# Kernel tuning notes

Measured on AMD Instinct MI355X. Metric: run time of the kernel, lower is better.

Reference implementation:

```python
import jax, jax.numpy as jnp
import numpy as np

D = 512        # d_model
DFF = 2048     # d_ffn
H = 8          # n_heads
L = 4          # n_blocks
EPS = 1e-5     # nn.LayerNorm default eps
NEG = -1e9


def _layer_norm(x, g, b):
    m = jnp.mean(x, axis=-1, keepdims=True)
    v = jnp.var(x, axis=-1, keepdims=True)
    return (x - m) / jnp.sqrt(v + EPS) * g + b


def setup_inputs() -> dict:
    key = jax.random.key(0)
    ks = jax.random.split(key, 6)
    B, S = 2, 2048
    s = 0.02
    x = jax.random.normal(ks[0], (B, S, D), dtype=jnp.float32)
    Wq = jax.random.normal(ks[1], (L, D, D), dtype=jnp.float32) * s
    Wk = jax.random.normal(ks[2], (L, D, D), dtype=jnp.float32) * s
    Wv = jax.random.normal(ks[3], (L, D, D), dtype=jnp.float32) * s
    W1 = jax.random.normal(ks[4], (L, D, DFF), dtype=jnp.float32) * s
    W2 = jax.random.normal(ks[5], (L, DFF, D), dtype=jnp.float32) * s
    z_d = jnp.zeros((L, D), dtype=jnp.float32)
    o_d = jnp.ones((L, D), dtype=jnp.float32)
    return {
        'x': x,
        'Wq': Wq, 'bq': z_d, 'Wk': Wk, 'bk': z_d, 'Wv': Wv, 'bv': z_d,
        'W1': W1, 'b1': jnp.zeros((L, DFF), dtype=jnp.float32),
        'W2': W2, 'b2': z_d,
        'g1': o_d, 'beta1': z_d, 'g2': o_d, 'beta2': z_d,
    }


def reference(x, Wq, bq, Wk, bk, Wv, bv, W1, b1, W2, b2, g1, beta1, g2, beta2):
    B, S, Dm = x.shape
    dk = Dm // H
    scale = 1.0 / (dk ** 0.5)

    def block(h, p):
        wq, bq_, wk, bk_, wv, bv_, w1, b1_, w2, b2_, g1_, be1, g2_, be2 = p
        # QKV projections, split heads: [B,S,D] -> [B,H,S,dk]
        q = (h @ wq + bq_).reshape(B, S, H, dk).transpose(0, 2, 1, 3)
        k = (h @ wk + bk_).reshape(B, S, H, dk).transpose(0, 2, 1, 3)
        v = (h @ wv + bv_).reshape(B, S, H, dk).transpose(0, 2, 1, 3)
        scores = jnp.einsum('bhqd,bhkd->bhqk', q, k) * scale
        # original quirk: padding=0, scores exactly equal to 0 get masked to -1e9
        scores = jnp.where(scores != 0, scores, NEG)
        probs = jax.nn.softmax(scores, axis=-1)
        attn = jnp.einsum('bhqk,bhkd->bhqd', probs, v)
        attn = attn.transpose(0, 2, 1, 3).reshape(B, S, Dm)
        h = _layer_norm(attn + h, g1_, be1)           # add_and_norm1
        ff = jax.nn.relu(h @ w1 + b1_) @ w2 + b2_     # position-wise FFN
        h = _layer_norm(h + ff, g2_, be2)             # add_and_norm2
        return h, None

    params = (Wq, bq, Wk, bk, Wv, bv, W1, b1, W2, b2, g1, beta1, g2, beta2)
    out, _ = jax.lax.scan(block, x, params)
    return out
```

## Files before the change

### kernel.cpp

```cpp
#include <hip/hip_runtime.h>
#include <stdint.h>
#include <math.h>


typedef __bf16 bf16_t;
typedef bf16_t bf16x8 __attribute__((ext_vector_type(8)));
typedef bf16_t bf16x4v __attribute__((ext_vector_type(4)));
typedef float  f32x4  __attribute__((ext_vector_type(4)));

__device__ __forceinline__ f32x4 mfma16(bf16x8 a, bf16x8 b, f32x4 c) {
    return __builtin_amdgcn_mfma_f32_16x16x32_bf16(a, b, c, 0, 0, 0);
}

__device__ __forceinline__ void cp16(const void* g, const void* l) {
    auto gp = reinterpret_cast<const __attribute__((address_space(1))) char*>(
        reinterpret_cast<uintptr_t>(g));
    auto lp = reinterpret_cast<__attribute__((address_space(3))) char*>(
        static_cast<uint32_t>(reinterpret_cast<uintptr_t>(l)));
    __builtin_amdgcn_global_load_lds((const __attribute__((address_space(1))) void*)gp,
                                     (__attribute__((address_space(3))) void*)lp,
                                     16, 0, 0);
}

__global__ void wconv_kernel(const float* __restrict__ Wq, const float* __restrict__ Wk,
                             const float* __restrict__ Wv, const float* __restrict__ W1,
                             const float* __restrict__ W2,
                             bf16_t* __restrict__ oQKV, bf16_t* __restrict__ oW1,
                             bf16_t* __restrict__ oW2)
{
    const int l = blockIdx.y;
    int t = blockIdx.x;
    const float* in; bf16_t* out; int Kd, Nd, tt;
    if (t < 192) {
        int m = t / 64; tt = t % 64; Kd = 512; Nd = 512;
        in  = (m == 0 ? Wq : m == 1 ? Wk : Wv) + (size_t)l * 512 * 512;
        out = oQKV + (size_t)l * 1536 * 512 + (size_t)m * 512 * 512;
    } else if (t < 448) {
        tt = t - 192; Kd = 512; Nd = 2048;
        in  = W1 + (size_t)l * 512 * 2048;
        out = oW1 + (size_t)l * 2048 * 512;
    } else {
        tt = t - 448; Kd = 2048; Nd = 512;
        in  = W2 + (size_t)l * 2048 * 512;
        out = oW2 + (size_t)l * 512 * 2048;
    }
    const int ntx = Nd >> 6;
    const int bk = (tt / ntx) * 64, bn = (tt % ntx) * 64;
    __shared__ float tile[64][65];
    const int tid = threadIdx.x;
    #pragma unroll
    for (int i = 0; i < 16; ++i) {
        int idx = i * 256 + tid; int r = idx >> 6, c = idx & 63;
        tile[r][c] = in[(size_t)(bk + r) * Nd + bn + c];
    }
    __syncthreads();
    #pragma unroll
    for (int i = 0; i < 4; ++i) {
        int idx = i * 256 + tid; int n = idx >> 4, kc = (idx & 15) * 4;
        bf16x4v o;
        o[0] = (bf16_t)tile[kc + 0][n];
        o[1] = (bf16_t)tile[kc + 1][n];
        o[2] = (bf16_t)tile[kc + 2][n];
        o[3] = (bf16_t)tile[kc + 3][n];
        *(bf16x4v*)&out[(size_t)(bn + n) * Kd + bk + kc] = o;
    }
}

__global__ void f2b_kernel(const float* __restrict__ in, bf16_t* __restrict__ out, int n)
{
    int i = (blockIdx.x * 256 + threadIdx.x) * 8;
    if (i >= n) return;
    float4 a = *(const float4*)(in + i);
    float4 b = *(const float4*)(in + i + 4);
    bf16x8 o;
    o[0] = (bf16_t)a.x; o[1] = (bf16_t)a.y; o[2] = (bf16_t)a.z; o[3] = (bf16_t)a.w;
    o[4] = (bf16_t)b.x; o[5] = (bf16_t)b.y; o[6] = (bf16_t)b.z; o[7] = (bf16_t)b.w;
    *(bf16x8*)(out + i) = o;
}

template<int MODE, bool RELU>
__global__ __launch_bounds__(256, 4) void gemm_kernel(
    const bf16_t* __restrict__ A, const bf16_t* __restrict__ Wt,
    const float* __restrict__ b0, const float* __restrict__ b1, const float* __restrict__ b2,
    void* __restrict__ o0, void* __restrict__ o1, void* __restrict__ o2,
    int N, int lda, int klen)
{
    __shared__ __align__(16) bf16_t lA[2][128 * 32];
    __shared__ __align__(16) bf16_t lB[2][128 * 32];
    const int tid = threadIdx.x;
    const int lane = tid & 63, w = tid >> 6;
    const int wm = w >> 1, wn = w & 1;
    const int l15 = lane & 15, quad = lane >> 4;
    const int row0 = blockIdx.y * 128, col0 = blockIdx.x * 128;
    const int kst = blockIdx.z * klen, kend = kst + klen;
    const int wbase = (tid & 192) * 16;

    f32x4 acc[4][4] = {};
    const char* Ab = (const char*)A;
    const char* Bb = (const char*)Wt;

    auto stage = [&](int k0, int buf) {
        #pragma unroll
        for (int p = 0; p < 2; ++p) {
            int o = (p * 256 + tid) * 16;
            int r = o >> 6, cb = o & 63;
            cp16(Ab + ((size_t)(row0 + r) * lda + k0) * 2 + cb, (char*)lA[buf] + p * 4096 + wbase);
            cp16(Bb + ((size_t)(col0 + r) * lda + k0) * 2 + cb, (char*)lB[buf] + p * 4096 + wbase);
        }
    };

    stage(kst, 0);
    int it = 0;
    for (int k0 = kst; k0 < kend; k0 += 32, ++it) {
        __syncthreads();
        if (k0 + 32 < kend) stage(k0 + 32, (it + 1) & 1);
        const bf16_t* cA = lA[it & 1];
        const bf16_t* cB = lB[it & 1];
        bf16x8 af[4], bv_[4];
        #pragma unroll
        for (int i = 0; i < 4; ++i)
            af[i] = *(const bf16x8*)&cA[(wm * 64 + i * 16 + l15) * 32 + quad * 8];
        #pragma unroll
        for (int i = 0; i < 4; ++i)
            bv_[i] = *(const bf16x8*)&cB[(wn * 64 + i * 16 + l15) * 32 + quad * 8];
        #pragma unroll
        for (int mi = 0; mi < 4; ++mi)
            #pragma unroll
            for (int ni = 0; ni < 4; ++ni)
                acc[mi][ni] = mfma16(af[mi], bv_[ni], acc[mi][ni]);
    }

    #pragma unroll
    for (int mi = 0; mi < 4; ++mi) {
        const int rowb = row0 + wm * 64 + mi * 16 + quad * 4;
        #pragma unroll
        for (int ni = 0; ni < 4; ++ni) {
            const int col = col0 + wn * 64 + ni * 16 + l15;
            if (MODE == 1) {
                const float bias = b0[col];
                #pragma unroll
                for (int r = 0; r < 4; ++r) {
                    float v = acc[mi][ni][r] + bias;
                    if (RELU) v = fmaxf(v, 0.f);
                    ((bf16_t*)o0)[(size_t)(rowb + r) * N + col] = (bf16_t)v;
                }
            } else if (MODE == 3) {
                bf16_t* op = (bf16_t*)o0 + (size_t)blockIdx.z * 4096 * 512;
                #pragma unroll
                for (int r = 0; r < 4; ++r)
                    op[(size_t)(rowb + r) * N + col] = (bf16_t)acc[mi][ni][r];
            } else {
                if (col < 512) {
                    const float bias = b0[col];
                    #pragma unroll
                    for (int r = 0; r < 4; ++r)
                        ((bf16_t*)o0)[(size_t)(rowb + r) * 512 + col] =
                            (bf16_t)((acc[mi][ni][r] + bias) * 0.18033688f);
                } else if (col < 1024) {
                    const int c = col - 512;
                    const float bias = b1[c];
                    #pragma unroll
                    for (int r = 0; r < 4; ++r)
                        ((bf16_t*)o1)[(size_t)(rowb + r) * 512 + c] =
                            (bf16_t)(acc[mi][ni][r] + bias);
                } else {
                    const int cv = col - 1024;
                    const int hh = cv >> 6, d = cv & 63;
                    const float bias = b2[cv];
                    const int b_ = rowb >> 11, s = rowb & 2047;
                    bf16x4v pk;
                    #pragma unroll
                    for (int r = 0; r < 4; ++r)
                        pk[r] = (bf16_t)(acc[mi][ni][r] + bias);
                    *(bf16x4v*)&((bf16_t*)o2)[(size_t)((b_ * 8 + hh) * 64 + d) * 2048 + s] = pk;
                }
            }
        }
    }
}

__global__ __launch_bounds__(256, 7) void attn_kernel(
    const bf16_t* __restrict__ Q, const bf16_t* __restrict__ Kg,
    const bf16_t* __restrict__ Vt, bf16_t* __restrict__ Op,
    float* __restrict__ Lb)
{
    __shared__ __align__(16) bf16_t lK[2][64 * 32];
    __shared__ __align__(16) bf16_t lV[2][64 * 32];
    __shared__ __align__(16) bf16_t lP[4][576];
    const int tid = threadIdx.x;
    const int lane = tid & 63, w = tid >> 6;
    const int l15 = lane & 15, quad = lane >> 4;
    const int bh = blockIdx.y, b = bh >> 3, h = bh & 7;
    const int q0 = blockIdx.x * 64;
    const int sp = blockIdx.z, kbase = sp * 512;
    const int wbase = w * 1024;
    const int srow = tid >> 2, scb = (tid & 3) * 16;

    bf16x8 qf[2];
    #pragma unroll
    for (int ks = 0; ks < 2; ++ks)
        qf[ks] = *(const bf16x8*)&Q[(size_t)(b * 2048 + q0 + w * 16 + l15) * 512
                                     + h * 64 + ks * 32 + quad * 8];

    f32x4 oaccT[4] = {};
    float tsum[4] = {0.f, 0.f, 0.f, 0.f};

    for (int t = 0; t < 8; ++t) {
        const int k0 = kbase + t * 64;
        __syncthreads();
        #pragma unroll
        for (int ks = 0; ks < 2; ++ks)
            cp16((const char*)Kg + ((size_t)(b * 2048 + k0 + srow) * 512 + h * 64 + ks * 32) * 2 + scb,
                 (char*)lK[ks] + wbase);
        #pragma unroll
        for (int g = 0; g < 2; ++g)
            cp16((const char*)Vt + ((size_t)(bh * 64 + srow) * 2048 + k0 + g * 32) * 2 + scb,
                 (char*)lV[g] + wbase);
        __syncthreads();

        f32x4 sacc[4] = {};
        #pragma unroll
        for (int ni = 0; ni < 4; ++ni) {
            bf16x8 kf0 = *(const bf16x8*)&lK[0][(ni * 16 + l15) * 32 + quad * 8];
            bf16x8 kf1 = *(const bf16x8*)&lK[1][(ni * 16 + l15) * 32 + quad * 8];
            sacc[ni] = mfma16(qf[0], kf0, sacc[ni]);
            sacc[ni] = mfma16(qf[1], kf1, sacc[ni]);
        }

        #pragma unroll
        for (int ni = 0; ni < 4; ++ni)
            #pragma unroll
            for (int r = 0; r < 4; ++r) {
                float s = sacc[ni][r];
                float p_ = (s == 0.f) ? 0.f : __builtin_amdgcn_exp2f(s);
                sacc[ni][r] = p_;
                tsum[r] += p_;
            }

        #pragma unroll
        for (int kc = 0; kc < 2; ++kc) {
            #pragma unroll
            for (int nn = 0; nn < 2; ++nn) {
                const int ni = kc * 2 + nn;
                #pragma unroll
                for (int r = 0; r < 4; ++r)
                    lP[w][(quad * 4 + r) * 36 + nn * 16 + l15] = (bf16_t)sacc[ni][r];
            }
            bf16x4v p0 = *(const bf16x4v*)&lP[w][l15 * 36 + quad * 8];
            bf16x4v p1 = *(const bf16x4v*)&lP[w][l15 * 36 + quad * 8 + 4];
            bf16x8 pf;
            #pragma unroll
            for (int j = 0; j < 4; ++j) { pf[j] = p0[j]; pf[4 + j] = p1[j]; }
            #pragma unroll
            for (int nd = 0; nd < 4; ++nd) {
                bf16x8 vf = *(const bf16x8*)&lV[kc][(nd * 16 + l15) * 32 + quad * 8];
                oaccT[nd] = mfma16(vf, pf, oaccT[nd]);
            }
        }
    }

    #pragma unroll
    for (int r = 0; r < 4; ++r) {
        float s_ = tsum[r];
        s_ += __shfl_xor(s_, 1);
        s_ += __shfl_xor(s_, 2);
        s_ += __shfl_xor(s_, 4);
        s_ += __shfl_xor(s_, 8);
        tsum[r] = s_;
    }

    bf16_t* op = Op + (size_t)sp * 4096 * 512;
    {
        const int row = b * 2048 + q0 + w * 16 + l15;
        #pragma unroll
        for (int nd = 0; nd < 4; ++nd) {
            bf16x4v pk;
            #pragma unroll
            for (int r = 0; r < 4; ++r) pk[r] = (bf16_t)oaccT[nd][r];
            *(bf16x4v*)&op[(size_t)row * 512 + h * 64 + nd * 16 + quad * 4] = pk;
        }
    }
    if (l15 == 0) {
        #pragma unroll
        for (int r = 0; r < 4; ++r) {
            int row = b * 2048 + q0 + w * 16 + quad * 4 + r;
            Lb[((size_t)row * 8 + h) * 4 + sp] = tsum[r];
        }
    }
}

__global__ void lnadd_c(const bf16_t* __restrict__ Op, const float* __restrict__ Lb,
                        const float* __restrict__ hin,
                        const float* __restrict__ g, const float* __restrict__ be,
                        float* __restrict__ Yf, bf16_t* __restrict__ Yb)
{
    const int row = blockIdx.x * 4 + (threadIdx.x >> 6);
    const int lane = threadIdx.x & 63;
    const int c0 = lane * 8;
    const int head = lane >> 3;
    const float4 l4 = *(const float4*)&Lb[((size_t)row * 8 + head) * 4];
    const float linv = 1.f / (l4.x + l4.y + l4.z + l4.w);
    const size_t idx = (size_t)row * 512 + c0;
    bf16x8 o0 = *(const bf16x8*)&Op[idx];
    bf16x8 o1 = *(const bf16x8*)&Op[idx + 2097152];
    bf16x8 o2 = *(const bf16x8*)&Op[idx + 2 * 2097152];
    bf16x8 o3 = *(const bf16x8*)&Op[idx + 3 * 2097152];
    float4 h0 = *(const float4*)&hin[idx];
    float4 h1 = *(const float4*)&hin[idx + 4];
    const float hr[8] = {h0.x, h0.y, h0.z, h0.w, h1.x, h1.y, h1.z, h1.w};
    float v[8]; float s = 0.f;
    #pragma unroll
    for (int j = 0; j < 8; ++j) {
        v[j] = ((float)o0[j] + (float)o1[j] + (float)o2[j] + (float)o3[j]) * linv + hr[j];
        s += v[j];
    }
    #pragma unroll
    for (int off = 32; off >= 1; off >>= 1) s += __shfl_xor(s, off);
    const float mean = s * (1.f / 512.f);
    float vs = 0.f;
    #pragma unroll
    for (int j = 0; j < 8; ++j) { float d = v[j] - mean; vs += d * d; }
    #pragma unroll
    for (int off = 32; off >= 1; off >>= 1) vs += __shfl_xor(vs, off);
    const float inv = rsqrtf(vs * (1.f / 512.f) + 1e-5f);
    float4 g0 = *(const float4*)&g[c0], g1 = *(const float4*)&g[c0 + 4];
    float4 b0 = *(const float4*)&be[c0], b1 = *(const float4*)&be[c0 + 4];
    const float gg[8] = {g0.x, g0.y, g0.z, g0.w, g1.x, g1.y, g1.z, g1.w};
    const float bb[8] = {b0.x, b0.y, b0.z, b0.w, b1.x, b1.y, b1.z, b1.w};
    float y[8]; bf16x8 yb;
    #pragma unroll
    for (int j = 0; j < 8; ++j) {
        y[j] = (v[j] - mean) * inv * gg[j] + bb[j];
        yb[j] = (bf16_t)y[j];
    }
    *(float4*)&Yf[idx]     = make_float4(y[0], y[1], y[2], y[3]);
    *(float4*)&Yf[idx + 4] = make_float4(y[4], y[5], y[6], y[7]);
    *(bf16x8*)&Yb[idx] = yb;
}

__global__ void lnadd_f(const bf16_t* __restrict__ G, const float* __restrict__ bias,
                        const float* __restrict__ hres, const float* __restrict__ g,
                        const float* __restrict__ be,
                        float* __restrict__ Yf, bf16_t* __restrict__ Yb)
{
    const int row = blockIdx.x * 4 + (threadIdx.x >> 6);
    const int lane = threadIdx.x & 63;
    const int c0 = lane * 8;
    const size_t idx = (size_t)row * 512 + c0;
    bf16x8 o0 = *(const bf16x8*)&G[idx];
    bf16x8 o1 = *(const bf16x8*)&G[idx + 2097152];
    bf16x8 o2 = *(const bf16x8*)&G[idx + 2 * 2097152];
    bf16x8 o3 = *(const bf16x8*)&G[idx + 3 * 2097152];
    float4 h0 = *(const float4*)&hres[idx];
    float4 h1 = *(const float4*)&hres[idx + 4];
    float4 bi0 = *(const float4*)&bias[c0], bi1 = *(const float4*)&bias[c0 + 4];
    const float hr[8] = {h0.x, h0.y, h0.z, h0.w, h1.x, h1.y, h1.z, h1.w};
    const float bs[8] = {bi0.x, bi0.y, bi0.z, bi0.w, bi1.x, bi1.y, bi1.z, bi1.w};
    float v[8]; float s = 0.f;
    #pragma unroll
    for (int j = 0; j < 8; ++j) {
        v[j] = (float)o0[j] + (float)o1[j] + (float)o2[j] + (float)o3[j] + bs[j] + hr[j];
        s += v[j];
    }
    #pragma unroll
    for (int off = 32; off >= 1; off >>= 1) s += __shfl_xor(s, off);
    const float mean = s * (1.f / 512.f);
    float vs = 0.f;
    #pragma unroll
    for (int j = 0; j < 8; ++j) { float d = v[j] - mean; vs += d * d; }
    #pragma unroll
    for (int off = 32; off >= 1; off >>= 1) vs += __shfl_xor(vs, off);
    const float inv = rsqrtf(vs * (1.f / 512.f) + 1e-5f);
    float4 g0 = *(const float4*)&g[c0], g1 = *(const float4*)&g[c0 + 4];
    float4 b0 = *(const float4*)&be[c0], b1 = *(const float4*)&be[c0 + 4];
    const float gg[8] = {g0.x, g0.y, g0.z, g0.w, g1.x, g1.y, g1.z, g1.w};
    const float bb[8] = {b0.x, b0.y, b0.z, b0.w, b1.x, b1.y, b1.z, b1.w};
    float y[8]; bf16x8 yb;
    #pragma unroll
    for (int j = 0; j < 8; ++j) {
        y[j] = (v[j] - mean) * inv * gg[j] + bb[j];
        yb[j] = (bf16_t)y[j];
    }
    *(float4*)&Yf[idx]     = make_float4(y[0], y[1], y[2], y[3]);
    *(float4*)&Yf[idx + 4] = make_float4(y[4], y[5], y[6], y[7]);
    *(bf16x8*)&Yb[idx] = yb;
}

extern "C" void kernel_launch(void* const* d_in, const int* in_sizes, int n_in,
                              void* d_out, int out_size, void* d_ws, size_t ws_size,
                              hipStream_t stream)
{
    const float* x   = (const float*)d_in[0];
    const float* Wq  = (const float*)d_in[1];
    const float* bq  = (const float*)d_in[2];
    const float* Wk  = (const float*)d_in[3];
    const float* bk  = (const float*)d_in[4];
    const float* Wv  = (const float*)d_in[5];
    const float* bv  = (const float*)d_in[6];
    const float* W1  = (const float*)d_in[7];
    const float* b1  = (const float*)d_in[8];
    const float* W2  = (const float*)d_in[9];
    const float* b2  = (const float*)d_in[10];
    const float* g1  = (const float*)d_in[11];
    const float* be1 = (const float*)d_in[12];
    const float* g2  = (const float*)d_in[13];
    const float* be2 = (const float*)d_in[14];

    char* p = (char*)d_ws;
    auto carve = [&](size_t bytes) { char* r = p; p += (bytes + 255) & ~(size_t)255; return r; };
    bf16_t* wQKV = (bf16_t*)carve(4UL * 1536 * 512 * 2);
    bf16_t* wW1t = (bf16_t*)carve(4UL * 2048 * 512 * 2);
    bf16_t* wW2t = (bf16_t*)carve(4UL * 512 * 2048 * 2);
    bf16_t* hbf  = (bf16_t*)carve(4096UL * 512 * 2);
    bf16_t* h2b  = (bf16_t*)carve(4096UL * 512 * 2);
    bf16_t* Fb   = (bf16_t*)carve(4096UL * 2048 * 2);
    bf16_t* R2   = (bf16_t*)carve(4UL * 4096 * 512 * 2);
    float*  Lbuf = (float*)carve(4096UL * 8 * 4 * 4);
    float*  h2f  = (float*)carve(4096UL * 512 * 4);
    float*  hf   = (float*)carve(4096UL * 512 * 4);
    bf16_t* Qb  = Fb;
    bf16_t* Kb  = Fb + 4096UL * 512;
    bf16_t* Vtb = Fb + 2UL * 4096 * 512;

    wconv_kernel<<<dim3(704, 4), 256, 0, stream>>>(Wq, Wk, Wv, W1, W2, wQKV, wW1t, wW2t);
    f2b_kernel<<<dim3(1024), 256, 0, stream>>>(x, hbf, 4096 * 512);

    const float* hin = x;
    for (int l = 0; l < 4; ++l) {
        gemm_kernel<2, false><<<dim3(12, 32, 1), 256, 0, stream>>>(
            hbf, wQKV + (size_t)l * 1536 * 512,
            bq + l * 512, bk + l * 512, bv + l * 512,
            Qb, Kb, Vtb, 1536, 512, 512);
        attn_kernel<<<dim3(32, 16, 4), 256, 0, stream>>>(Qb, Kb, Vtb, R2, Lbuf);
        lnadd_c<<<dim3(1024), 256, 0, stream>>>(R2, Lbuf, hin,
                                                g1 + l * 512, be1 + l * 512, h2f, h2b);
        gemm_kernel<1, true><<<dim3(16, 32, 1), 256, 0, stream>>>(
            h2b, wW1t + (size_t)l * 2048 * 512,
            b1 + l * 2048, nullptr, nullptr,
            Fb, nullptr, nullptr, 2048, 512, 512);
        gemm_kernel<3, false><<<dim3(4, 32, 4), 256, 0, stream>>>(
            Fb, wW2t + (size_t)l * 512 * 2048,
            nullptr, nullptr, nullptr,
            R2, nullptr, nullptr, 512, 2048, 512);
        float* yout = (l == 3) ? (float*)d_out : hf;
        lnadd_f<<<dim3(1024), 256, 0, stream>>>(R2, b2 + l * 512, h2f,
                                                g2 + l * 512, be2 + l * 512, yout, hbf);
        hin = hf;
    }
    (void)in_sizes; (void)n_in; (void)out_size; (void)ws_size;
}
```

Before: 526.8 us.

## Double attention query tile per block to reuse K/V tiles across two row groups

Each attention block now handles 128 query rows instead of 64, with every wave computing two 16-row MFMA tiles that share the K and V fragments loaded from LDS. The aim is to halve the global-to-LDS K/V traffic and the LDS fragment reads per query, and to spread the barrier cost over more work. The grid is remapped so that the batch-head and key-split indices come from blockIdx.x, which changes the order in which blocks are scheduled. In exchange, register and LDS use per block go up, launch bounds drop from 7 to 4 waves, and the grid has half as many blocks (1024).

```diff
diff --git a/kernel.cpp b/kernel.cpp
--- a/kernel.cpp
+++ b/kernel.cpp
@@ -179,31 +179,34 @@
     }
 }
 
-__global__ __launch_bounds__(256, 7) void attn_kernel(
+__global__ __launch_bounds__(256, 4) void attn_kernel(
     const bf16_t* __restrict__ Q, const bf16_t* __restrict__ Kg,
     const bf16_t* __restrict__ Vt, bf16_t* __restrict__ Op,
     float* __restrict__ Lb)
 {
     __shared__ __align__(16) bf16_t lK[2][64 * 32];
     __shared__ __align__(16) bf16_t lV[2][64 * 32];
-    __shared__ __align__(16) bf16_t lP[4][576];
+    __shared__ __align__(16) bf16_t lP[4][1152];
     const int tid = threadIdx.x;
     const int lane = tid & 63, w = tid >> 6;
     const int l15 = lane & 15, quad = lane >> 4;
-    const int bh = blockIdx.y, b = bh >> 3, h = bh & 7;
-    const int q0 = blockIdx.x * 64;
-    const int sp = blockIdx.z, kbase = sp * 512;
+    const int bh = blockIdx.x & 15, sp = blockIdx.x >> 4;
+    const int b = bh >> 3, h = bh & 7;
+    const int q0 = blockIdx.y * 128;
+    const int kbase = sp * 512;
     const int wbase = w * 1024;
     const int srow = tid >> 2, scb = (tid & 3) * 16;
 
-    bf16x8 qf[2];
-    #pragma unroll
-    for (int ks = 0; ks < 2; ++ks)
-        qf[ks] = *(const bf16x8*)&Q[(size_t)(b * 2048 + q0 + w * 16 + l15) * 512
-                                     + h * 64 + ks * 32 + quad * 8];
-
-    f32x4 oaccT[4] = {};
-    float tsum[4] = {0.f, 0.f, 0.f, 0.f};
+    bf16x8 qf[2][2];
+    #pragma unroll
+    for (int mi = 0; mi < 2; ++mi)
+        #pragma unroll
+        for (int ks = 0; ks < 2; ++ks)
+            qf[mi][ks] = *(const bf16x8*)&Q[(size_t)(b * 2048 + q0 + w * 32 + mi * 16 + l15) * 512
+                                            + h * 64 + ks * 32 + quad * 8];
+
+    f32x4 oaccT[2][4] = {};
+    float tsum[2][4] = {};
 
     for (int t = 0; t < 8; ++t) {
         const int k0 = kbase + t * 64;
@@ -218,73 +221,87 @@
                  (char*)lV[g] + wbase);
         __syncthreads();
 
-        f32x4 sacc[4] = {};
+        f32x4 sacc[2][4] = {};
         #pragma unroll
         for (int ni = 0; ni < 4; ++ni) {
             bf16x8 kf0 = *(const bf16x8*)&lK[0][(ni * 16 + l15) * 32 + quad * 8];
             bf16x8 kf1 = *(const bf16x8*)&lK[1][(ni * 16 + l15) * 32 + quad * 8];
-            sacc[ni] = mfma16(qf[0], kf0, sacc[ni]);
-            sacc[ni] = mfma16(qf[1], kf1, sacc[ni]);
-        }
-
-        #pragma unroll
-        for (int ni = 0; ni < 4; ++ni)
-            #pragma unroll
-            for (int r = 0; r < 4; ++r) {
-                float s = sacc[ni][r];
-                float p_ = (s == 0.f) ? 0.f : __builtin_amdgcn_exp2f(s);
-                sacc[ni][r] = p_;
-                tsum[r] += p_;
+            sacc[0][ni] = mfma16(qf[0][0], kf0, sacc[0][ni]);
+            sacc[0][ni] = mfma16(qf[0][1], kf1, sacc[0][ni]);
+            sacc[1][ni] = mfma16(qf[1][0], kf0, sacc[1][ni]);
+            sacc[1][ni] = mfma16(qf[1][1], kf1, sacc[1][ni]);
+        }
+
+        #pragma unroll
+        for (int mi = 0; mi < 2; ++mi)
+            #pragma unroll
+            for (int ni = 0; ni < 4; ++ni)
+                #pragma unroll
+                for (int r = 0; r < 4; ++r) {
+                    float s = sacc[mi][ni][r];
+                    float p_ = (s == 0.f) ? 0.f : __builtin_amdgcn_exp2f(s);
+                    sacc[mi][ni][r] = p_;
+                    tsum[mi][r] += p_;
+                }
+
+        #pragma unroll
+        for (int kc = 0; kc < 2; ++kc) {
+            #pragma unroll
+            for (int mi = 0; mi < 2; ++mi)
+                #pragma unroll
+                for (int nn = 0; nn < 2; ++nn) {
+                    const int ni = kc * 2 + nn;
+                    #pragma unroll
+                    for (int r = 0; r < 4; ++r)
+                        lP[w][(mi * 16 + quad * 4 + r) * 36 + nn * 16 + l15] =
+                            (bf16_t)sacc[mi][ni][r];
+                }
+            bf16x8 pf[2];
+            #pragma unroll
+            for (int mi = 0; mi < 2; ++mi) {
+                bf16x4v p0 = *(const bf16x4v*)&lP[w][(mi * 16 + l15) * 36 + quad * 8];
+                bf16x4v p1 = *(const bf16x4v*)&lP[w][(mi * 16 + l15) * 36 + quad * 8 + 4];
+                #pragma unroll
+                for (int j = 0; j < 4; ++j) { pf[mi][j] = p0[j]; pf[mi][4 + j] = p1[j]; }
             }
-
-        #pragma unroll
-        for (int kc = 0; kc < 2; ++kc) {
-            #pragma unroll
-            for (int nn = 0; nn < 2; ++nn) {
-                const int ni = kc * 2 + nn;
-                #pragma unroll
-                for (int r = 0; r < 4; ++r)
-                    lP[w][(quad * 4 + r) * 36 + nn * 16 + l15] = (bf16_t)sacc[ni][r];
-            }
-            bf16x4v p0 = *(const bf16x4v*)&lP[w][l15 * 36 + quad * 8];
-            bf16x4v p1 = *(const bf16x4v*)&lP[w][l15 * 36 + quad * 8 + 4];
-            bf16x8 pf;
-            #pragma unroll
-            for (int j = 0; j < 4; ++j) { pf[j] = p0[j]; pf[4 + j] = p1[j]; }
             #pragma unroll
             for (int nd = 0; nd < 4; ++nd) {
                 bf16x8 vf = *(const bf16x8*)&lV[kc][(nd * 16 + l15) * 32 + quad * 8];
-                oaccT[nd] = mfma16(vf, pf, oaccT[nd]);
+                oaccT[0][nd] = mfma16(vf, pf[0], oaccT[0][nd]);
+                oaccT[1][nd] = mfma16(vf, pf[1], oaccT[1][nd]);
             }
         }
     }
 
     #pragma unroll
-    for (int r = 0; r < 4; ++r) {
-        float s_ = tsum[r];
-        s_ += __shfl_xor(s_, 1);
-        s_ += __shfl_xor(s_, 2);
-        s_ += __shfl_xor(s_, 4);
-        s_ += __shfl_xor(s_, 8);
-        tsum[r] = s_;
-    }
+    for (int mi = 0; mi < 2; ++mi)
+        #pragma unroll
+        for (int r = 0; r < 4; ++r) {
+            float s_ = tsum[mi][r];
+            s_ += __shfl_xor(s_, 1);
+            s_ += __shfl_xor(s_, 2);
+            s_ += __shfl_xor(s_, 4);
+            s_ += __shfl_xor(s_, 8);
+            tsum[mi][r] = s_;
+        }
 
     bf16_t* op = Op + (size_t)sp * 4096 * 512;
-    {
-        const int row = b * 2048 + q0 + w * 16 + l15;
+    #pragma unroll
+    for (int mi = 0; mi < 2; ++mi) {
+        const int row = b * 2048 + q0 + w * 32 + mi * 16 + l15;
         #pragma unroll
         for (int nd = 0; nd < 4; ++nd) {
             bf16x4v pk;
             #pragma unroll
-            for (int r = 0; r < 4; ++r) pk[r] = (bf16_t)oaccT[nd][r];
+            for (int r = 0; r < 4; ++r) pk[r] = (bf16_t)oaccT[mi][nd][r];
             *(bf16x4v*)&op[(size_t)row * 512 + h * 64 + nd * 16 + quad * 4] = pk;
         }
-    }
-    if (l15 == 0) {
-        #pragma unroll
-        for (int r = 0; r < 4; ++r) {
-            int row = b * 2048 + q0 + w * 16 + quad * 4 + r;
-            Lb[((size_t)row * 8 + h) * 4 + sp] = tsum[r];
+        if (l15 == 0) {
+            #pragma unroll
+            for (int r = 0; r < 4; ++r) {
+                int rr = b * 2048 + q0 + w * 32 + mi * 16 + quad * 4 + r;
+                Lb[((size_t)rr * 8 + h) * 4 + sp] = tsum[mi][r];
+            }
         }
     }
 }
@@ -431,7 +448,7 @@
             hbf, wQKV + (size_t)l * 1536 * 512,
             bq + l * 512, bk + l * 512, bv + l * 512,
             Qb, Kb, Vtb, 1536, 512, 512);
-        attn_kernel<<<dim3(32, 16, 4), 256, 0, stream>>>(Qb, Kb, Vtb, R2, Lbuf);
+        attn_kernel<<<dim3(64, 16), 256, 0, stream>>>(Qb, Kb, Vtb, R2, Lbuf);
         lnadd_c<<<dim3(1024), 256, 0, stream>>>(R2, Lbuf, hin,
                                                 g1 + l * 512, be1 + l * 512, h2f, h2b);
         gemm_kernel<1, true><<<dim3(16, 32, 1), 256, 0, stream>>>(
```

Result: faster. 506.6 us, median of 3 (-3.8%).
